# Optimization experiments

Hardware: AMD Instinct MI355X
Metric: run time of the kernel (lower is better)

The kernel has to match this reference:

```python
import jax, jax.numpy as jnp
import numpy as np

G, T, D_IN, D_OUT = 8, 4096, 1024, 4096


def setup_inputs() -> dict:
    key = jax.random.key(0)
    k1, k2, k3 = jax.random.split(key, 3)
    x = jax.random.normal(k1, (T, D_IN), dtype=jnp.float32)
    # cumulative end offsets per group: sorted, last == T (grouped_mm convention)
    cuts = jnp.sort(jax.random.randint(k2, (G - 1,), 0, T, dtype=jnp.int32))
    offs = jnp.concatenate([cuts, jnp.array([T], dtype=jnp.int32)])
    weight = jax.random.normal(k3, (G, D_OUT, D_IN), dtype=jnp.float32) * (D_IN ** -0.5)
    return {"input": x, "grouped_mm_offs": offs, "weight": weight}


def reference(input, grouped_mm_offs, weight):
    # Grouped GEMM: row t (with offs[g-1] <= t < offs[g]) -> input[t] @ weight[g].T
    n_tok = input.shape[0]
    tok = jnp.arange(n_tok)
    gid = jnp.searchsorted(grouped_mm_offs, tok, side="right")  # [T] group id per row
    # Dense all-expert projection [G, T, D_OUT], then select the routed expert per row.
    proj = jnp.einsum("ti,goi->gto", input, weight)
    return proj[gid, tok]  # [T, D_OUT]
```

## Files before the change

### kernel.cpp

```cpp
#include <hip/hip_runtime.h>
#include <hip/hip_bf16.h>

#define NG 8
#define NT 4096
#define DIN 1024
#define DOUT 4096
#define BM 256
#define BN 128
#define BK 64
#define KTILES (DIN / BK)
#define NTILES (DOUT / BN)
#define RTILES (NT / BM + NG)
#define ATILESZ (BM * BK * 2)
#define BTILESZ (BN * BK * 2)

typedef __attribute__((ext_vector_type(4))) float f32x4;
typedef __attribute__((ext_vector_type(8))) short bf16x8;

__device__ __forceinline__ void gld16(const void* g, void* l) {
    __builtin_amdgcn_global_load_lds(
        (const __attribute__((address_space(1))) void*)(g),
        (__attribute__((address_space(3))) void*)(l), 16, 0, 0);
}

__device__ __forceinline__ unsigned long long pack4bf(f32x4 v) {
    union { __hip_bfloat16 h; unsigned short u; } c0, c1, c2, c3;
    c0.h = __float2bfloat16(v[0]);
    c1.h = __float2bfloat16(v[1]);
    c2.h = __float2bfloat16(v[2]);
    c3.h = __float2bfloat16(v[3]);
    return (unsigned long long)c0.u | ((unsigned long long)c1.u << 16) |
           ((unsigned long long)c2.u << 32) | ((unsigned long long)c3.u << 48);
}

__device__ __forceinline__ int swz(int row, int colb) {
    return row * 128 + (colb ^ ((row & 7) << 4));
}

__global__ __launch_bounds__(256)
void cvt_x_kernel(const float* __restrict__ x, short* __restrict__ xb) {
    const int n4 = NT * DIN / 4;
    for (int i = blockIdx.x * blockDim.x + threadIdx.x; i < n4;
         i += gridDim.x * blockDim.x) {
        f32x4 v = ((const f32x4*)x)[i];
        ((unsigned long long*)xb)[i] = pack4bf(v);
    }
}

__global__ __launch_bounds__(256, 2)
void grouped_gemm_bf16(const short* __restrict__ xb,
                       const int* __restrict__ offs,
                       const float* __restrict__ w,
                       float* __restrict__ out) {
    __shared__ char lds[2 * ATILESZ + BTILESZ];
    char* ldsB = lds + 2 * ATILESZ;

    const int rt = blockIdx.y;
    const int n0 = blockIdx.x * BN;
    int row0 = 0, endg = 0, gsel = -1;
    {
        int acc = 0, prev = 0;
        for (int g = 0; g < NG; ++g) {
            int e = offs[g];
            int cnt = (e - prev + BM - 1) / BM;
            if (rt < acc + cnt) { gsel = g; row0 = prev + (rt - acc) * BM; endg = e; break; }
            acc += cnt; prev = e;
        }
    }
    if (gsel < 0) return;
    const float* wg = w + (size_t)gsel * DOUT * DIN;

    const int tid  = threadIdx.x;
    const int lane = tid & 63;
    const int wid  = tid >> 6;
    const int wrM  = wid >> 1, wcN = wid & 1;
    const int lrow = lane & 15, kgrp = lane >> 4;

    int axoff[8], sbaseA[8];
    #pragma unroll
    for (int i = 0; i < 8; ++i) {
        int stripe = i * 4 + wid;
        int r = stripe * 8 + (lane >> 3);
        int cs = (lane & 7) ^ (r & 7);
        int ar = row0 + r; if (ar >= endg) ar = endg - 1;
        axoff[i]  = ar * DIN + cs * 8;
        sbaseA[i] = stripe * 1024;
    }
    const int sr = tid >> 4, sc4 = tid & 15;
    int boff[8];
    #pragma unroll
    for (int i = 0; i < 8; ++i) boff[i] = (n0 + sr + i * 16) * DIN + sc4 * 4;

    f32x4 acc[8][4];
    #pragma unroll
    for (int m = 0; m < 8; ++m)
        #pragma unroll
        for (int n = 0; n < 4; ++n)
            acc[m][n] = (f32x4){0.f, 0.f, 0.f, 0.f};

    f32x4 pB[8];

    #pragma unroll
    for (int i = 0; i < 8; ++i) gld16(xb + axoff[i], lds + sbaseA[i]);
    #pragma unroll
    for (int i = 0; i < 8; ++i) pB[i] = *(const f32x4*)(wg + boff[i]);
    #pragma unroll
    for (int i = 0; i < 8; ++i)
        *(unsigned long long*)(ldsB + swz(sr + i * 16, sc4 * 8)) = pack4bf(pB[i]);
    asm volatile("s_waitcnt vmcnt(0) lgkmcnt(0)" ::: "memory");
    __builtin_amdgcn_sched_barrier(0);
    __builtin_amdgcn_s_barrier();
    __builtin_amdgcn_sched_barrier(0);

    for (int kt = 0; kt < KTILES; ++kt) {
        const int cur = kt & 1;
        const char* lA = lds + cur * ATILESZ;

        if (kt + 1 < KTILES) {
            const int k0 = (kt + 1) * BK;
            #pragma unroll
            for (int i = 0; i < 8; ++i) pB[i] = *(const f32x4*)(wg + boff[i] + k0);
            #pragma unroll
            for (int i = 0; i < 8; ++i)
                gld16(xb + axoff[i] + k0, lds + (cur ^ 1) * ATILESZ + sbaseA[i]);
            __builtin_amdgcn_sched_barrier(0);
        }

        __builtin_amdgcn_s_setprio(1);
        #pragma unroll
        for (int kk = 0; kk < 2; ++kk) {
            const int kb = kk * 64 + kgrp * 16;
            bf16x8 af[8], bb[4];
            #pragma unroll
            for (int m = 0; m < 8; ++m) {
                int r = wrM * 128 + m * 16 + lrow;
                af[m] = *(const bf16x8*)(lA + r * 128 + (((kb >> 4) ^ (r & 7)) << 4));
            }
            #pragma unroll
            for (int n = 0; n < 4; ++n)
                bb[n] = *(const bf16x8*)(ldsB + swz(wcN * 64 + n * 16 + lrow, kb));
            #pragma unroll
            for (int m = 0; m < 8; ++m)
                #pragma unroll
                for (int n = 0; n < 4; ++n)
                    acc[m][n] = __builtin_amdgcn_mfma_f32_16x16x32_bf16(
                        af[m], bb[n], acc[m][n], 0, 0, 0);
        }
        __builtin_amdgcn_s_setprio(0);

        if (kt + 1 < KTILES) {
            __builtin_amdgcn_sched_barrier(0);
            __builtin_amdgcn_s_barrier();
            __builtin_amdgcn_sched_barrier(0);

            #pragma unroll
            for (int i = 0; i < 8; ++i)
                *(unsigned long long*)(ldsB + swz(sr + i * 16, sc4 * 8)) = pack4bf(pB[i]);

            asm volatile("s_waitcnt vmcnt(0) lgkmcnt(0)" ::: "memory");
            __builtin_amdgcn_sched_barrier(0);
            __builtin_amdgcn_s_barrier();
            __builtin_amdgcn_sched_barrier(0);
        }
    }

    #pragma unroll
    for (int m = 0; m < 8; ++m) {
        #pragma unroll
        for (int j = 0; j < 4; ++j) {
            int row = row0 + wrM * 128 + m * 16 + kgrp * 4 + j;
            if (row < endg) {
                #pragma unroll
                for (int n = 0; n < 4; ++n) {
                    int col = n0 + wcN * 64 + n * 16 + lrow;
                    out[(size_t)row * DOUT + col] = acc[m][n][j];
                }
            }
        }
    }
}

extern "C" void kernel_launch(void* const* d_in, const int* in_sizes, int n_in,
                              void* d_out, int out_size, void* d_ws, size_t ws_size,
                              hipStream_t stream) {
    const float* x    = (const float*)d_in[0];
    const int*   offs = (const int*)d_in[1];
    const float* w    = (const float*)d_in[2];
    float* out = (float*)d_out;
    short* xb  = (short*)d_ws;

    cvt_x_kernel<<<1024, 256, 0, stream>>>(x, xb);
    dim3 grid(NTILES, RTILES, 1);
    grouped_gemm_bf16<<<grid, 256, 0, stream>>>(xb, offs, w, out);
}
```

Before: 81.51 us.

## Split grouped GEMM into 8-wave, 4-phase pipelined k-loop with double-buffered B

```diff
diff --git a/kernel.cpp b/kernel.cpp
--- a/kernel.cpp
+++ b/kernel.cpp
@@ -11,6 +11,7 @@
 #define KTILES (DIN / BK)
 #define NTILES (DOUT / BN)
 #define RTILES (NT / BM + NG)
+#define THREADS 512
 #define ATILESZ (BM * BK * 2)
 #define BTILESZ (BN * BK * 2)
 
@@ -47,24 +48,25 @@
     }
 }
 
-__global__ __launch_bounds__(256, 2)
-void grouped_gemm_bf16(const short* __restrict__ xb,
-                       const int* __restrict__ offs,
-                       const float* __restrict__ w,
-                       float* __restrict__ out) {
-    __shared__ char lds[2 * ATILESZ + BTILESZ];
+__global__ __launch_bounds__(THREADS, 2)
+void grouped_gemm_8ph(const short* __restrict__ xb,
+                      const int* __restrict__ offs,
+                      const float* __restrict__ w,
+                      float* __restrict__ out) {
+    __shared__ char lds[2 * ATILESZ + 2 * BTILESZ];
+    char* ldsA = lds;
     char* ldsB = lds + 2 * ATILESZ;
 
     const int rt = blockIdx.y;
     const int n0 = blockIdx.x * BN;
     int row0 = 0, endg = 0, gsel = -1;
     {
-        int acc = 0, prev = 0;
+        int acc0 = 0, prev = 0;
         for (int g = 0; g < NG; ++g) {
             int e = offs[g];
             int cnt = (e - prev + BM - 1) / BM;
-            if (rt < acc + cnt) { gsel = g; row0 = prev + (rt - acc) * BM; endg = e; break; }
-            acc += cnt; prev = e;
+            if (rt < acc0 + cnt) { gsel = g; row0 = prev + (rt - acc0) * BM; endg = e; break; }
+            acc0 += cnt; prev = e;
         }
     }
     if (gsel < 0) return;
@@ -73,13 +75,14 @@
     const int tid  = threadIdx.x;
     const int lane = tid & 63;
     const int wid  = tid >> 6;
-    const int wrM  = wid >> 1, wcN = wid & 1;
+    const int wrM  = wid >> 2;
+    const int wcN  = wid & 3;
     const int lrow = lane & 15, kgrp = lane >> 4;
 
-    int axoff[8], sbaseA[8];
-    #pragma unroll
-    for (int i = 0; i < 8; ++i) {
-        int stripe = i * 4 + wid;
+    int axoff[4], sbaseA[4];
+    #pragma unroll
+    for (int i = 0; i < 4; ++i) {
+        int stripe = wid + i * 8;
         int r = stripe * 8 + (lane >> 3);
         int cs = (lane & 7) ^ (r & 7);
         int ar = row0 + r; if (ar >= endg) ar = endg - 1;
@@ -87,80 +90,112 @@
         sbaseA[i] = stripe * 1024;
     }
     const int sr = tid >> 4, sc4 = tid & 15;
-    int boff[8];
-    #pragma unroll
-    for (int i = 0; i < 8; ++i) boff[i] = (n0 + sr + i * 16) * DIN + sc4 * 4;
-
-    f32x4 acc[8][4];
+    int boff[4];
+    #pragma unroll
+    for (int i = 0; i < 4; ++i) boff[i] = (n0 + sr + i * 32) * DIN + sc4 * 4;
+
+    f32x4 acc[8][2];
     #pragma unroll
     for (int m = 0; m < 8; ++m)
         #pragma unroll
-        for (int n = 0; n < 4; ++n)
+        for (int n = 0; n < 2; ++n)
             acc[m][n] = (f32x4){0.f, 0.f, 0.f, 0.f};
 
-    f32x4 pB[8];
-
-    #pragma unroll
-    for (int i = 0; i < 8; ++i) gld16(xb + axoff[i], lds + sbaseA[i]);
-    #pragma unroll
-    for (int i = 0; i < 8; ++i) pB[i] = *(const f32x4*)(wg + boff[i]);
-    #pragma unroll
-    for (int i = 0; i < 8; ++i)
-        *(unsigned long long*)(ldsB + swz(sr + i * 16, sc4 * 8)) = pack4bf(pB[i]);
-    asm volatile("s_waitcnt vmcnt(0) lgkmcnt(0)" ::: "memory");
-    __builtin_amdgcn_sched_barrier(0);
-    __builtin_amdgcn_s_barrier();
-    __builtin_amdgcn_sched_barrier(0);
+    f32x4 pB[4];
+
+    #pragma unroll
+    for (int i = 0; i < 4; ++i) pB[i] = *(const f32x4*)(wg + boff[i]);
+    #pragma unroll
+    for (int i = 0; i < 4; ++i) gld16(xb + axoff[i], ldsA + sbaseA[i]);
+    #pragma unroll
+    for (int i = 0; i < 4; ++i)
+        *(unsigned long long*)(ldsB + swz(sr + i * 32, sc4 * 8)) = pack4bf(pB[i]);
 
     for (int kt = 0; kt < KTILES; ++kt) {
         const int cur = kt & 1;
-        const char* lA = lds + cur * ATILESZ;
+        const char* lA = ldsA + cur * ATILESZ;
+        const char* lB = ldsB + cur * BTILESZ;
 
         if (kt + 1 < KTILES) {
             const int k0 = (kt + 1) * BK;
             #pragma unroll
-            for (int i = 0; i < 8; ++i) pB[i] = *(const f32x4*)(wg + boff[i] + k0);
-            #pragma unroll
-            for (int i = 0; i < 8; ++i)
-                gld16(xb + axoff[i] + k0, lds + (cur ^ 1) * ATILESZ + sbaseA[i]);
-            __builtin_amdgcn_sched_barrier(0);
-        }
-
-        __builtin_amdgcn_s_setprio(1);
+            for (int i = 0; i < 4; ++i) pB[i] = *(const f32x4*)(wg + boff[i] + k0);
+            #pragma unroll
+            for (int i = 0; i < 4; ++i)
+                gld16(xb + axoff[i] + k0, ldsA + (cur ^ 1) * ATILESZ + sbaseA[i]);
+            __builtin_amdgcn_sched_barrier(0);
+            asm volatile("s_waitcnt vmcnt(8) lgkmcnt(0)" ::: "memory");
+        } else {
+            __builtin_amdgcn_sched_barrier(0);
+            asm volatile("s_waitcnt vmcnt(0) lgkmcnt(0)" ::: "memory");
+        }
+        __builtin_amdgcn_sched_barrier(0);
+        __builtin_amdgcn_s_barrier();
+        __builtin_amdgcn_sched_barrier(0);
+
+        bf16x8 bb[2][2];
+        {
+            #pragma unroll
+            for (int n = 0; n < 2; ++n)
+                #pragma unroll
+                for (int kk = 0; kk < 2; ++kk)
+                    bb[n][kk] = *(const bf16x8*)(lB + swz(wcN * 32 + n * 16 + lrow,
+                                                          kk * 64 + kgrp * 16));
+            bf16x8 af[2][2];
+            #pragma unroll
+            for (int q = 0; q < 2; ++q)
+                #pragma unroll
+                for (int kk = 0; kk < 2; ++kk) {
+                    int rA = wrM * 128 + q * 16 + lrow;
+                    int kb = kk * 64 + kgrp * 16;
+                    af[q][kk] = *(const bf16x8*)(lA + rA * 128 + ((((kb >> 4) ^ (rA & 7))) << 4));
+                }
+            asm volatile("s_waitcnt lgkmcnt(0)" ::: "memory");
+            __builtin_amdgcn_sched_barrier(0);
+            __builtin_amdgcn_s_setprio(1);
+            #pragma unroll
+            for (int q = 0; q < 2; ++q)
+                #pragma unroll
+                for (int n = 0; n < 2; ++n)
+                    #pragma unroll
+                    for (int kk = 0; kk < 2; ++kk)
+                        acc[q][n] = __builtin_amdgcn_mfma_f32_16x16x32_bf16(
+                            af[q][kk], bb[n][kk], acc[q][n], 0, 0, 0);
+            __builtin_amdgcn_s_setprio(0);
+            __builtin_amdgcn_s_barrier();
+        }
+
         #pragma unroll
-        for (int kk = 0; kk < 2; ++kk) {
-            const int kb = kk * 64 + kgrp * 16;
-            bf16x8 af[8], bb[4];
-            #pragma unroll
-            for (int m = 0; m < 8; ++m) {
-                int r = wrM * 128 + m * 16 + lrow;
-                af[m] = *(const bf16x8*)(lA + r * 128 + (((kb >> 4) ^ (r & 7)) << 4));
+        for (int p = 1; p < 4; ++p) {
+            bf16x8 af[2][2];
+            #pragma unroll
+            for (int q = 0; q < 2; ++q)
+                #pragma unroll
+                for (int kk = 0; kk < 2; ++kk) {
+                    int rA = wrM * 128 + (2 * p + q) * 16 + lrow;
+                    int kb = kk * 64 + kgrp * 16;
+                    af[q][kk] = *(const bf16x8*)(lA + rA * 128 + ((((kb >> 4) ^ (rA & 7))) << 4));
+                }
+            if (p == 3 && kt + 1 < KTILES) {
+                #pragma unroll
+                for (int i = 0; i < 4; ++i)
+                    *(unsigned long long*)(ldsB + (cur ^ 1) * BTILESZ +
+                                           swz(sr + i * 32, sc4 * 8)) = pack4bf(pB[i]);
             }
-            #pragma unroll
-            for (int n = 0; n < 4; ++n)
-                bb[n] = *(const bf16x8*)(ldsB + swz(wcN * 64 + n * 16 + lrow, kb));
-            #pragma unroll
-            for (int m = 0; m < 8; ++m)
-                #pragma unroll
-                for (int n = 0; n < 4; ++n)
-                    acc[m][n] = __builtin_amdgcn_mfma_f32_16x16x32_bf16(
-                        af[m], bb[n], acc[m][n], 0, 0, 0);
-        }
-        __builtin_amdgcn_s_setprio(0);
-
-        if (kt + 1 < KTILES) {
-            __builtin_amdgcn_sched_barrier(0);
             __builtin_amdgcn_s_barrier();
-            __builtin_amdgcn_sched_barrier(0);
-
-            #pragma unroll
-            for (int i = 0; i < 8; ++i)
-                *(unsigned long long*)(ldsB + swz(sr + i * 16, sc4 * 8)) = pack4bf(pB[i]);
-
-            asm volatile("s_waitcnt vmcnt(0) lgkmcnt(0)" ::: "memory");
-            __builtin_amdgcn_sched_barrier(0);
+            asm volatile("s_waitcnt lgkmcnt(0)" ::: "memory");
+            __builtin_amdgcn_sched_barrier(0);
+            __builtin_amdgcn_s_setprio(1);
+            #pragma unroll
+            for (int q = 0; q < 2; ++q)
+                #pragma unroll
+                for (int n = 0; n < 2; ++n)
+                    #pragma unroll
+                    for (int kk = 0; kk < 2; ++kk)
+                        acc[2 * p + q][n] = __builtin_amdgcn_mfma_f32_16x16x32_bf16(
+                            af[q][kk], bb[n][kk], acc[2 * p + q][n], 0, 0, 0);
+            __builtin_amdgcn_s_setprio(0);
             __builtin_amdgcn_s_barrier();
-            __builtin_amdgcn_sched_barrier(0);
         }
     }
 
@@ -171,8 +206,8 @@
             int row = row0 + wrM * 128 + m * 16 + kgrp * 4 + j;
             if (row < endg) {
                 #pragma unroll
-                for (int n = 0; n < 4; ++n) {
-                    int col = n0 + wcN * 64 + n * 16 + lrow;
+                for (int n = 0; n < 2; ++n) {
+                    int col = n0 + wcN * 32 + n * 16 + lrow;
                     out[(size_t)row * DOUT + col] = acc[m][n][j];
                 }
             }
@@ -191,5 +226,5 @@
 
     cvt_x_kernel<<<1024, 256, 0, stream>>>(x, xb);
     dim3 grid(NTILES, RTILES, 1);
-    grouped_gemm_bf16<<<grid, 256, 0, stream>>>(xb, offs, w, out);
-}
+    grouped_gemm_8ph<<<grid, THREADS, 0, stream>>>(xb, offs, w, out);
+}
```

Result: slower. 90.08 us (+10.5%).
